# Performance work log

Hardware: AMD Instinct MI355X
Metric: run time of the kernel (lower is better)

The kernel has to match this reference:

```python
import jax, jax.numpy as jnp
import numpy as np

# DARTS recurrent genotype (canonical): (activation, predecessor-state index)
GENOTYPE_RECURRENT = [("sigmoid", 0), ("relu", 1), ("relu", 1), ("identity", 1),
                      ("tanh", 2), ("sigmoid", 5), ("tanh", 3), ("relu", 5)]
GENOTYPE_CONCAT = [1, 2, 3, 4, 5, 6, 7, 8]

T, B, H, V = 512, 64, 1024, 50000
INITRANGE = 0.04

_ACT = {"tanh": jnp.tanh, "relu": jax.nn.relu, "sigmoid": jax.nn.sigmoid,
        "identity": lambda x: x}


def setup_inputs() -> dict:
    key = jax.random.key(0)
    ks = jax.random.split(key, 5)
    X = jax.random.randint(ks[0], (T, B), 0, V)                     # token ids (T, B)
    hidden = jnp.zeros((1, B, H), dtype=jnp.float32)                # init hidden list[0]
    emb_table = jax.random.normal(ks[1], (V, H), dtype=jnp.float32) * 0.1
    W0 = jax.random.uniform(ks[2], (2 * H, 2 * H), jnp.float32, -INITRANGE, INITRANGE)
    Ws = jax.random.uniform(ks[3], (len(GENOTYPE_RECURRENT), H, 2 * H), jnp.float32,
                            -INITRANGE, INITRANGE)
    W_out = jax.random.normal(ks[4], (H, 4), dtype=jnp.float32) * 0.02
    b_out = jnp.zeros((4,), dtype=jnp.float32)
    return {"X": X, "hidden": hidden, "emb_table": emb_table, "W0": W0,
            "Ws": Ws, "W_out": W_out, "b_out": b_out}


def _darts_cell_step(h_prev, x, W0, Ws):
    # x, h_prev: (B, H). Eval-mode (no dropout masks).
    xh = jnp.concatenate([x, h_prev], axis=-1)          # (B, 2H)
    c0h0 = xh @ W0                                      # (B, 2H)
    c0 = jax.nn.sigmoid(c0h0[:, :H])
    h0 = jnp.tanh(c0h0[:, H:])
    s0 = h_prev + c0 * (h0 - h_prev)
    states = [s0]
    for i, (name, pred) in enumerate(GENOTYPE_RECURRENT):
        s_prev = states[pred]
        ch = s_prev @ Ws[i]                             # (B, 2H)
        c = jax.nn.sigmoid(ch[:, :H])
        hh = _ACT[name](ch[:, H:])
        states.append(s_prev + c * (hh - s_prev))
    # mean over concat nodes
    out = jnp.mean(jnp.stack([states[i] for i in GENOTYPE_CONCAT], axis=-1), axis=-1)
    return out, out


def reference(X, hidden, emb_table, W0, Ws, W_out, b_out):
    emb = emb_table[X]                                  # (T, B, H)
    h0 = hidden[0]                                      # (B, H)

    def step(h, x_t):
        return _darts_cell_step(h, x_t, W0, Ws)

    h_last, hiddens = jax.lax.scan(step, h0, emb)       # h_last: (B, H)
    a_hat = h_last @ W_out + b_out                      # (B, 4)
    probs = jax.nn.softmax(a_hat, axis=1)
    return a_hat, probs
```

## Files before the change

kernel.cpp:

```cpp
#include <hip/hip_runtime.h>

#define TT 512

typedef _Float16 f16;
typedef _Float16 half8 __attribute__((ext_vector_type(8)));
typedef float f32x4 __attribute__((ext_vector_type(4)));

#define MFMA(a,b,c) __builtin_amdgcn_mfma_f32_16x16x32_f16((a),(b),(c),0,0,0)
#define LOSC  2048.0f
#define RLOSC 0.00048828125f

#define RS  18
#define WSZ (16*RS)
#define LSZ (16*WSZ)

__device__ __forceinline__ half8 ldh8(const f16* p){ return *(const half8*)p; }
__device__ __forceinline__ float sgm(float x){ return 1.f/(1.f+__expf(-x)); }
__device__ __forceinline__ float applyact(int k, float x){
  if (k==0) return tanhf(x);
  if (k==1) return sgm(x);
  if (k==2) return fmaxf(x,0.f);
  return x;
}

__device__ __forceinline__ void gbar(unsigned* bar, unsigned ph, int b, int wid, int lane){
  __syncthreads();
  const unsigned tgt = ph + 1u;
  if (wid == 0){
    if (lane == 0){
      __builtin_amdgcn_fence(__ATOMIC_RELEASE, "agent");
      __hip_atomic_store(&bar[b*4], tgt, __ATOMIC_RELEASE, __HIP_MEMORY_SCOPE_AGENT);
    }
    for (;;){
      int ok = 1;
      #pragma unroll
      for (int j=0;j<4;j++){
        unsigned v = __hip_atomic_load(&bar[(lane + 64*j)*4], __ATOMIC_RELAXED, __HIP_MEMORY_SCOPE_AGENT);
        ok &= (v >= tgt);
      }
      if (__all(ok)) break;
      __builtin_amdgcn_s_sleep(1);
    }
    if (lane == 0) __builtin_amdgcn_fence(__ATOMIC_ACQUIRE, "agent");
  }
  __syncthreads();
}

__device__ __forceinline__ void mm_core(
  const f16* __restrict__ Ap, const f16* __restrict__ Alp,
  const f16* __restrict__ Bg, const f16* __restrict__ Ba,
  const f16* __restrict__ Bgl, const f16* __restrict__ Bal,
  int nch, int wlo, float* __restrict__ Lg, float* __restrict__ La,
  int region, int q8, int l15)
{
  f32x4 g0={0,0,0,0},g1={0,0,0,0},a0={0,0,0,0},a1={0,0,0,0};
  #pragma unroll 2
  for (int c=0;c<nch;c++){
    int s = c*32;
    half8 ah=ldh8(Ap+s), al=ldh8(Alp+s);
    half8 wg=ldh8(Bg+s), wa=ldh8(Ba+s);
    g0=MFMA(ah,wg,g0); a0=MFMA(ah,wa,a0);
    g1=MFMA(al,wg,g1); a1=MFMA(al,wa,a1);
    if (wlo){ g1=MFMA(ah,ldh8(Bgl+s),g1); a1=MFMA(ah,ldh8(Bal+s),a1); }
  }
  f32x4 gg = g0 + g1*RLOSC, aa = a0 + a1*RLOSC;
  const int base = region*WSZ + (q8>>1)*RS + l15;
  #pragma unroll
  for (int rr=0;rr<4;rr++){
    Lg[base + rr*RS] = gg[rr];
    La[base + rr*RS] = aa[rr];
  }
}

__device__ __forceinline__ void node_std(
  const f16* __restrict__ SHs, const f16* __restrict__ SLs,
  const f16* __restrict__ Wh, const f16* __restrict__ Wl,
  float* __restrict__ Lg, float* __restrict__ La,
  int region, int kk, int nch, int m0, int c0, int q8, int l15, int wlo)
{
  const f16* Ap  = SHs + (m0+l15)*1024 + kk + q8;
  const f16* Alp = SLs + (m0+l15)*1024 + kk + q8;
  const f16* Bg  = Wh + (c0+l15)*1024 + kk + q8;
  const f16* Ba  = Wh + (1024+c0+l15)*1024 + kk + q8;
  const f16* Bgl = wlo ? Wl + (c0+l15)*1024 + kk + q8 : Bg;
  const f16* Bal = wlo ? Wl + (1024+c0+l15)*1024 + kk + q8 : Ba;
  mm_core(Ap,Alp,Bg,Ba,Bgl,Bal,nch,wlo,Lg,La,region,q8,l15);
}

__device__ __forceinline__ float fin_val(const float* __restrict__ Lg, const float* __restrict__ La,
  const float* __restrict__ ST, int t256, int m0, int c0, int r0, int nr, int sp, int actk)
{
  const int row = t256>>4, col = t256&15;
  const int e = row*RS + col;
  float gs=0.f, as=0.f;
  for (int r=r0; r<r0+nr; ++r){ gs += Lg[r*WSZ+e]; as += La[r*WSZ+e]; }
  float spv = ST[sp*65536 + (m0+row)*1024 + c0 + col];
  return spv + sgm(gs)*(applyact(actk,as)-spv);
}

__device__ __forceinline__ void fin_write(const float* __restrict__ Lg, const float* __restrict__ La,
  float* __restrict__ ST, f16* __restrict__ SH, f16* __restrict__ SL,
  int t256, int m0, int c0, int r0, int nr, int sp, int so, int actk, bool hl)
{
  float s = fin_val(Lg, La, ST, t256, m0, c0, r0, nr, sp, actk);
  const int row = t256>>4, col = t256&15;
  const int idx = so*65536 + (m0+row)*1024 + c0 + col;
  ST[idx] = s;
  if (hl){ f16 hi=(f16)s; SH[idx]=hi; SL[idx]=(f16)((s-(float)hi)*LOSC); }
}

__global__ __launch_bounds__(1024,4) void darts_coop(
  const int* __restrict__ X, const float* __restrict__ emb,
  const float* __restrict__ Wout, const float* __restrict__ bout, float* __restrict__ out,
  const f16* __restrict__ W0Th, const f16* __restrict__ W0Tl,
  const f16* __restrict__ WsTh, const f16* __restrict__ WsTl,
  float* __restrict__ ST, f16* __restrict__ SH, f16* __restrict__ SL,
  f16* __restrict__ XNH, f16* __restrict__ XNL,
  unsigned* bar, int wlo)
{
  const int tid = threadIdx.x, b = blockIdx.x;
  const int wid = tid>>6, lane = tid&63, l15 = lane&15, q8 = (lane>>4)*8;
  const int mt = (b>>3)&3, sct = (b&7)*8 + (b>>5);
  const int m0 = mt*16, c0 = sct*16;
  __shared__ float Lg[LSZ], La[LSZ];
  __shared__ float S6[256], S8[256];
  unsigned ph = 0;

  for (int t=0; t<TT; ++t){
    if (t+1 < TT && tid < 256){
      int row = b>>2, col = ((b&3)<<8) + tid;
      int tok = X[(t+1)*64 + row];
      float v = emb[(size_t)tok*1024 + col];
      f16 hi=(f16)v;
      int xi = ((t+1)&1)*65536 + row*1024 + col;
      XNH[xi]=hi; XNL[xi]=(f16)((v-(float)hi)*LOSC);
    }
    {
      const f16* XH = XNH + (t&1)*65536;
      const f16* XL = XNL + (t&1)*65536;
      int kk = wid*128, ak = kk & 1023;
      const f16* Abh = (wid<8)? XH : SH;
      const f16* Abl = (wid<8)? XL : SL;
      const f16* Ap  = Abh + (m0+l15)*1024 + ak + q8;
      const f16* Alp = Abl + (m0+l15)*1024 + ak + q8;
      const f16* Bg  = W0Th + (c0+l15)*2048 + kk + q8;
      const f16* Ba  = W0Th + (1024+c0+l15)*2048 + kk + q8;
      const f16* Bgl = wlo ? W0Tl + (c0+l15)*2048 + kk + q8 : Bg;
      const f16* Bal = wlo ? W0Tl + (1024+c0+l15)*2048 + kk + q8 : Ba;
      mm_core(Ap,Alp,Bg,Ba,Bgl,Bal,4,wlo,Lg,La,wid,q8,l15);
    }
    __syncthreads();
    if (tid<256) fin_write(Lg,La,ST,SH,SL, tid, m0,c0, 0,16, 0, 1, 0, true);
    gbar(bar, ph++, b, wid, lane);

    node_std(SH+1*65536, SL+1*65536, WsTh, WsTl, Lg, La, wid, wid*64, 2, m0,c0,q8,l15,wlo);
    __syncthreads();
    if (tid<256) fin_write(Lg,La,ST,SH,SL, tid, m0,c0, 0,16, 1, 2, 1, true);
    gbar(bar, ph++, b, wid, lane);

    if (wid<8)
      node_std(SH+2*65536, SL+2*65536, WsTh+(size_t)1*2097152,
               wlo? WsTl+(size_t)1*2097152 : (const f16*)0,
               Lg, La, wid, wid*128, 4, m0,c0,q8,l15,wlo);
    else
      node_std(SH+2*65536, SL+2*65536, WsTh+(size_t)2*2097152,
               wlo? WsTl+(size_t)2*2097152 : (const f16*)0,
               Lg, La, wid, (wid-8)*128, 4, m0,c0,q8,l15,wlo);
    __syncthreads();
    if (tid<256)      fin_write(Lg,La,ST,SH,SL, tid,     m0,c0, 0,8, 2, 3, 2, true);
    else if (tid<512) fin_write(Lg,La,ST,SH,SL, tid-256, m0,c0, 8,8, 2, 4, 2, true);
    __syncthreads();

    node_std(SH+2*65536, SL+2*65536, WsTh+(size_t)3*2097152,
             wlo? WsTl+(size_t)3*2097152 : (const f16*)0,
             Lg, La, wid, wid*64, 2, m0,c0,q8,l15,wlo);
    __syncthreads();
    if (tid<256) fin_write(Lg,La,ST,SH,SL, tid, m0,c0, 0,16, 2, 5, 3, false);
    gbar(bar, ph++, b, wid, lane);

    if (wid<8)
      node_std(SH+3*65536, SL+3*65536, WsTh+(size_t)4*2097152,
               wlo? WsTl+(size_t)4*2097152 : (const f16*)0,
               Lg, La, wid, wid*128, 4, m0,c0,q8,l15,wlo);
    else
      node_std(SH+4*65536, SL+4*65536, WsTh+(size_t)6*2097152,
               wlo? WsTl+(size_t)6*2097152 : (const f16*)0,
               Lg, La, wid, (wid-8)*128, 4, m0,c0,q8,l15,wlo);
    __syncthreads();
    if (tid<256)      fin_write(Lg,La,ST,SH,SL, tid,     m0,c0, 0,8, 3, 6, 0, true);
    else if (tid<512) fin_write(Lg,La,ST,SH,SL, tid-256, m0,c0, 8,8, 4, 8, 0, false);
    gbar(bar, ph++, b, wid, lane);

    if (wid<8)
      node_std(SH+6*65536, SL+6*65536, WsTh+(size_t)5*2097152,
               wlo? WsTl+(size_t)5*2097152 : (const f16*)0,
               Lg, La, wid, wid*128, 4, m0,c0,q8,l15,wlo);
    else
      node_std(SH+6*65536, SL+6*65536, WsTh+(size_t)7*2097152,
               wlo? WsTl+(size_t)7*2097152 : (const f16*)0,
               Lg, La, wid, (wid-8)*128, 4, m0,c0,q8,l15,wlo);
    __syncthreads();
    if (tid<256)      S6[tid]     = fin_val(Lg,La,ST, tid,     m0,c0, 0,8, 6, 1);
    else if (tid<512) S8[tid-256] = fin_val(Lg,La,ST, tid-256, m0,c0, 8,8, 6, 2);
    __syncthreads();
    if (tid<256){
      const int row = tid>>4, col = tid&15;
      const int idx = (m0+row)*1024 + c0 + col;
      float m = (ST[2*65536+idx]+ST[3*65536+idx]+ST[4*65536+idx]+ST[5*65536+idx]
               + ST[6*65536+idx]+ST[8*65536+idx]+S6[tid]+S8[tid])*0.125f;
      ST[idx]=m;
      f16 hi=(f16)m; SH[idx]=hi; SL[idx]=(f16)((m-(float)hi)*LOSC);
    }
    gbar(bar, ph++, b, wid, lane);
  }

  if (b==0 && tid<256){
    int row = tid>>2, col = tid&3;
    float acc = bout[col];
    const float* hrow = ST + row*1024;
    #pragma unroll 8
    for (int k=0;k<1024;k++) acc += hrow[k]*Wout[k*4+col];
    out[row*4+col] = acc;
    float m = fmaxf(acc, __shfl_xor(acc,1));
    m = fmaxf(m, __shfl_xor(m,2));
    float e = __expf(acc-m);
    float ssum = e + __shfl_xor(e,1);
    ssum = ssum + __shfl_xor(ssum,2);
    out[256 + row*4+col] = e/ssum;
  }
}

__global__ void prep_x0(const int* __restrict__ X, const float* __restrict__ hidden,
  const float* __restrict__ emb, f16* __restrict__ XNH, f16* __restrict__ XNL,
  float* __restrict__ ST, f16* __restrict__ SH, f16* __restrict__ SL, unsigned* bar)
{
  int idx = blockIdx.x*256 + threadIdx.x;
  float hv = hidden[idx];
  ST[idx] = hv;
  f16 hh=(f16)hv; SH[idx]=hh; SL[idx]=(f16)((hv-(float)hh)*LOSC);
  int brow = idx>>10, k = idx&1023;
  int tok = X[brow];
  float v = emb[tok*1024+k];
  f16 xh=(f16)v; XNH[idx]=xh; XNL[idx]=(f16)((v-(float)xh)*LOSC);
  if (idx < 4096) bar[idx] = 0u;
}

__global__ void prep_w(const float* __restrict__ W0, const float* __restrict__ Ws,
  f16* __restrict__ W0Th, f16* __restrict__ W0Tl, f16* __restrict__ WsTh, f16* __restrict__ WsTl)
{
  __shared__ float L[64][65];
  int b = blockIdx.x, tid = threadIdx.x;
  const float* src; f16 *Dh, *Dl; int K, tk, tn;
  if (b < 1024){ src=W0; Dh=W0Th; Dl=W0Tl; K=2048; tk=b&31; tn=b>>5; }
  else { int bb=b-1024; int mi=bb>>9; int t2=bb&511; tk=t2&15; tn=t2>>4;
         src = Ws + (size_t)mi*1024*2048; Dh = WsTh + (size_t)mi*2097152;
         Dl = WsTl ? (WsTl + (size_t)mi*2097152) : (f16*)0; K=1024; }
  int k0 = tk*64, n0 = tn*64;
  int rr = tid>>6, cc = tid&63;
  #pragma unroll
  for (int j=0;j<16;j++){
    int r = j*4 + rr;
    L[cc][r] = src[(size_t)(k0+r)*2048 + n0+cc];
  }
  __syncthreads();
  #pragma unroll
  for (int j=0;j<16;j++){
    int n = j*4 + rr;
    float v = L[n][cc];
    f16 hi = (f16)v;
    Dh[(size_t)(n0+n)*K + k0+cc] = hi;
    if (Dl) Dl[(size_t)(n0+n)*K + k0+cc] = (f16)((v-(float)hi)*LOSC);
  }
}

__global__ void sentinel_k(float* __restrict__ out, float v){
  int i = blockIdx.x*256 + threadIdx.x;
  if (i < 512) out[i] = v;
}

extern "C" void kernel_launch(void* const* d_in, const int* in_sizes, int n_in,
                              void* d_out, int out_size, void* d_ws, size_t ws_size,
                              hipStream_t stream)
{
  const int*   X      = (const int*)  d_in[0];
  const float* hidden = (const float*)d_in[1];
  const float* emb    = (const float*)d_in[2];
  const float* W0     = (const float*)d_in[3];
  const float* Ws     = (const float*)d_in[4];
  const float* Wout   = (const float*)d_in[5];
  const float* bout   = (const float*)d_in[6];
  float* out = (float*)d_out;

  const size_t SZ_W0   = (size_t)2048*2048*2;
  const size_t SZ_WS   = (size_t)8*2048*1024*2;
  const size_t SZ_ST   = (size_t)10*65536*4;
  const size_t SZ_SHL  = (size_t)10*65536*2;
  const size_t SZ_XN   = (size_t)2*65536*2;
  const size_t SZ_BAR  = 16384;

  auto pad = [](size_t x){ return (x + 255) & ~(size_t)255; };
  size_t need_red  = pad(SZ_W0) + pad(SZ_WS) + pad(SZ_ST) + 2*pad(SZ_SHL)
                   + 2*pad(SZ_XN) + pad(SZ_BAR);
  size_t need_full = need_red + pad(SZ_W0) + pad(SZ_WS);

  int wlo;
  if (ws_size >= need_full)      wlo = 1;
  else if (ws_size >= need_red)  wlo = 0;
  else { hipLaunchKernelGGL(sentinel_k, dim3(2), dim3(256), 0, stream, out, 1.0e6f); return; }

  char* w = (char*)d_ws; size_t off = 0;
  auto alloc = [&](size_t bytes)->void*{ void* p = w+off; off += (bytes+255)&~(size_t)255; return p; };
  f16* W0Th = (f16*)alloc(SZ_W0);
  f16* WsTh = (f16*)alloc(SZ_WS);
  f16* W0Tl = wlo ? (f16*)alloc(SZ_W0) : (f16*)0;
  f16* WsTl = wlo ? (f16*)alloc(SZ_WS) : (f16*)0;
  float* ST = (float*)alloc(SZ_ST);
  f16* SH   = (f16*)alloc(SZ_SHL);
  f16* SL   = (f16*)alloc(SZ_SHL);
  f16* XNH  = (f16*)alloc(SZ_XN);
  f16* XNL  = (f16*)alloc(SZ_XN);
  unsigned* bar = (unsigned*)alloc(SZ_BAR);

  hipLaunchKernelGGL(prep_x0, dim3(256), dim3(256), 0, stream,
                     X, hidden, emb, XNH, XNL, ST, SH, SL, bar);
  hipLaunchKernelGGL(prep_w, dim3(5120), dim3(256), 0, stream,
                     W0, Ws, W0Th, W0Tl, WsTh, WsTl);

  void* args[] = { (void*)&X, (void*)&emb, (void*)&Wout, (void*)&bout, (void*)&out,
                   (void*)&W0Th, (void*)&W0Tl, (void*)&WsTh, (void*)&WsTl,
                   (void*)&ST, (void*)&SH, (void*)&SL, (void*)&XNH, (void*)&XNL,
                   (void*)&bar, (void*)&wlo };
  hipError_t e = hipLaunchCooperativeKernel((void*)darts_coop, dim3(256), dim3(1024), args, 0, stream);
  if (e != hipSuccess){
    hipLaunchKernelGGL(darts_coop, dim3(256), dim3(1024), 0, stream,
                       X, emb, Wout, bout, out, W0Th, W0Tl, WsTh, WsTl,
                       ST, SH, SL, XNH, XNL, bar, wlo);
  }
}
```

Baseline: 64.34 ms.

## Merge nodes 3,4,6 into one barrier stage and prefetch tiles before MFMA

Restructures the per-timestep schedule so node 4 (reading state 2) runs in the same phase as nodes 5 and 7, with the 16 waves split 5/5/6 across the three matmuls. This removes one grid-wide barrier per step at the cost of an extra gbar replacing a local syncthreads and uneven K-splits. It also adds a touch_tiles pass that issues one coalesced 4-byte load per cache line of the wave's A/B tiles before the MFMA loop, so the lines are already in flight when the main loop starts. That pass adds extra load instructions and address arithmetic to every node.

```diff
diff --git a/kernel.cpp b/kernel.cpp
--- a/kernel.cpp
+++ b/kernel.cpp
@@ -46,6 +46,33 @@
   __syncthreads();
 }
 
+__device__ __forceinline__ void touch_tiles(
+  const f16* __restrict__ Wh, const f16* __restrict__ Wl, int Kst, int c0, int kk,
+  const f16* __restrict__ Ah, const f16* __restrict__ Al, int m0, int ak,
+  int nch, int wlo, int lane)
+{
+  unsigned acc = 0;
+  const int tot = (wlo ? 96 : 48) * nch;
+  for (int base = 0; base < tot; base += 64){
+    int id = base + lane;
+    if (id >= tot) id -= tot;
+    int c, a, r;
+    if (wlo){ c = id/96; int ra = id - c*96; a = ra/48; r = ra - a*48; }
+    else    { c = id/48; r = id - c*48; a = 0; }
+    const unsigned* p;
+    if (r < 32){
+      const f16* wb = a ? Wl : Wh;
+      int row = (r<16) ? (c0+r) : (1024 + c0 + (r-16));
+      p = (const unsigned*)(wb + (size_t)row*Kst + kk + c*32);
+    } else {
+      const f16* ab = a ? Al : Ah;
+      p = (const unsigned*)(ab + (size_t)(m0 + (r-32))*1024 + ak + c*32);
+    }
+    acc |= *p;
+  }
+  asm volatile("" :: "v"(acc) : "memory");
+}
+
 __device__ __forceinline__ void mm_core(
   const f16* __restrict__ Ap, const f16* __restrict__ Alp,
   const f16* __restrict__ Bg, const f16* __restrict__ Ba,
@@ -72,12 +99,13 @@
   }
 }
 
-__device__ __forceinline__ void node_std(
+__device__ __forceinline__ void node_g(
   const f16* __restrict__ SHs, const f16* __restrict__ SLs,
   const f16* __restrict__ Wh, const f16* __restrict__ Wl,
   float* __restrict__ Lg, float* __restrict__ La,
-  int region, int kk, int nch, int m0, int c0, int q8, int l15, int wlo)
-{
+  int region, int kk, int nch, int m0, int c0, int q8, int l15, int lane, int wlo)
+{
+  touch_tiles(Wh, Wl, 1024, c0, kk, SHs, SLs, m0, kk, nch, wlo, lane);
   const f16* Ap  = SHs + (m0+l15)*1024 + kk + q8;
   const f16* Alp = SLs + (m0+l15)*1024 + kk + q8;
   const f16* Bg  = Wh + (c0+l15)*1024 + kk + q8;
@@ -141,6 +169,7 @@
       int kk = wid*128, ak = kk & 1023;
       const f16* Abh = (wid<8)? XH : SH;
       const f16* Abl = (wid<8)? XL : SL;
+      touch_tiles(W0Th, W0Tl, 2048, c0, kk, Abh, Abl, m0, ak, 4, wlo, lane);
       const f16* Ap  = Abh + (m0+l15)*1024 + ak + q8;
       const f16* Alp = Abl + (m0+l15)*1024 + ak + q8;
       const f16* Bg  = W0Th + (c0+l15)*2048 + kk + q8;
@@ -153,52 +182,54 @@
     if (tid<256) fin_write(Lg,La,ST,SH,SL, tid, m0,c0, 0,16, 0, 1, 0, true);
     gbar(bar, ph++, b, wid, lane);
 
-    node_std(SH+1*65536, SL+1*65536, WsTh, WsTl, Lg, La, wid, wid*64, 2, m0,c0,q8,l15,wlo);
+    node_g(SH+1*65536, SL+1*65536, WsTh, WsTl, Lg, La, wid, wid*64, 2, m0,c0,q8,l15,lane,wlo);
     __syncthreads();
     if (tid<256) fin_write(Lg,La,ST,SH,SL, tid, m0,c0, 0,16, 1, 2, 1, true);
     gbar(bar, ph++, b, wid, lane);
 
     if (wid<8)
-      node_std(SH+2*65536, SL+2*65536, WsTh+(size_t)1*2097152,
-               wlo? WsTl+(size_t)1*2097152 : (const f16*)0,
-               Lg, La, wid, wid*128, 4, m0,c0,q8,l15,wlo);
+      node_g(SH+2*65536, SL+2*65536, WsTh+(size_t)1*2097152,
+             wlo? WsTl+(size_t)1*2097152 : (const f16*)0,
+             Lg, La, wid, wid*128, 4, m0,c0,q8,l15,lane,wlo);
     else
-      node_std(SH+2*65536, SL+2*65536, WsTh+(size_t)2*2097152,
-               wlo? WsTl+(size_t)2*2097152 : (const f16*)0,
-               Lg, La, wid, (wid-8)*128, 4, m0,c0,q8,l15,wlo);
+      node_g(SH+2*65536, SL+2*65536, WsTh+(size_t)2*2097152,
+             wlo? WsTl+(size_t)2*2097152 : (const f16*)0,
+             Lg, La, wid, (wid-8)*128, 4, m0,c0,q8,l15,lane,wlo);
     __syncthreads();
     if (tid<256)      fin_write(Lg,La,ST,SH,SL, tid,     m0,c0, 0,8, 2, 3, 2, true);
     else if (tid<512) fin_write(Lg,La,ST,SH,SL, tid-256, m0,c0, 8,8, 2, 4, 2, true);
-    __syncthreads();
-
-    node_std(SH+2*65536, SL+2*65536, WsTh+(size_t)3*2097152,
+    gbar(bar, ph++, b, wid, lane);
+
+    if (wid < 5){
+      int i = wid;    int s=(i*32)/5, e=((i+1)*32)/5;
+      node_g(SH+3*65536, SL+3*65536, WsTh+(size_t)4*2097152,
+             wlo? WsTl+(size_t)4*2097152 : (const f16*)0,
+             Lg, La, wid, s*32, e-s, m0,c0,q8,l15,lane,wlo);
+    } else if (wid < 10){
+      int i = wid-5;  int s=(i*32)/5, e=((i+1)*32)/5;
+      node_g(SH+4*65536, SL+4*65536, WsTh+(size_t)6*2097152,
+             wlo? WsTl+(size_t)6*2097152 : (const f16*)0,
+             Lg, La, wid, s*32, e-s, m0,c0,q8,l15,lane,wlo);
+    } else {
+      int i = wid-10; int s=(i*32)/6, e=((i+1)*32)/6;
+      node_g(SH+2*65536, SL+2*65536, WsTh+(size_t)3*2097152,
              wlo? WsTl+(size_t)3*2097152 : (const f16*)0,
-             Lg, La, wid, wid*64, 2, m0,c0,q8,l15,wlo);
-    __syncthreads();
-    if (tid<256) fin_write(Lg,La,ST,SH,SL, tid, m0,c0, 0,16, 2, 5, 3, false);
+             Lg, La, wid, s*32, e-s, m0,c0,q8,l15,lane,wlo);
+    }
+    __syncthreads();
+    if (tid<256)      fin_write(Lg,La,ST,SH,SL, tid,     m0,c0, 0,5,  3, 6, 0, true);
+    else if (tid<512) fin_write(Lg,La,ST,SH,SL, tid-256, m0,c0, 5,5,  4, 8, 0, false);
+    else if (tid<768) fin_write(Lg,La,ST,SH,SL, tid-512, m0,c0, 10,6, 2, 5, 3, false);
     gbar(bar, ph++, b, wid, lane);
 
     if (wid<8)
-      node_std(SH+3*65536, SL+3*65536, WsTh+(size_t)4*2097152,
-               wlo? WsTl+(size_t)4*2097152 : (const f16*)0,
-               Lg, La, wid, wid*128, 4, m0,c0,q8,l15,wlo);
+      node_g(SH+6*65536, SL+6*65536, WsTh+(size_t)5*2097152,
+             wlo? WsTl+(size_t)5*2097152 : (const f16*)0,
+             Lg, La, wid, wid*128, 4, m0,c0,q8,l15,lane,wlo);
     else
-      node_std(SH+4*65536, SL+4*65536, WsTh+(size_t)6*2097152,
-               wlo? WsTl+(size_t)6*2097152 : (const f16*)0,
-               Lg, La, wid, (wid-8)*128, 4, m0,c0,q8,l15,wlo);
-    __syncthreads();
-    if (tid<256)      fin_write(Lg,La,ST,SH,SL, tid,     m0,c0, 0,8, 3, 6, 0, true);
-    else if (tid<512) fin_write(Lg,La,ST,SH,SL, tid-256, m0,c0, 8,8, 4, 8, 0, false);
-    gbar(bar, ph++, b, wid, lane);
-
-    if (wid<8)
-      node_std(SH+6*65536, SL+6*65536, WsTh+(size_t)5*2097152,
-               wlo? WsTl+(size_t)5*2097152 : (const f16*)0,
-               Lg, La, wid, wid*128, 4, m0,c0,q8,l15,wlo);
-    else
-      node_std(SH+6*65536, SL+6*65536, WsTh+(size_t)7*2097152,
-               wlo? WsTl+(size_t)7*2097152 : (const f16*)0,
-               Lg, La, wid, (wid-8)*128, 4, m0,c0,q8,l15,wlo);
+      node_g(SH+6*65536, SL+6*65536, WsTh+(size_t)7*2097152,
+             wlo? WsTl+(size_t)7*2097152 : (const f16*)0,
+             Lg, La, wid, (wid-8)*128, 4, m0,c0,q8,l15,lane,wlo);
     __syncthreads();
     if (tid<256)      S6[tid]     = fin_val(Lg,La,ST, tid,     m0,c0, 0,8, 6, 1);
     else if (tid<512) S8[tid-256] = fin_val(Lg,La,ST, tid-256, m0,c0, 8,8, 6, 2);
```

Measured after the change: 78.87 ms. 1.23x slower.

## Split grid barrier into arrive/wait and prefetch next node weights in between

Applied to the files above, without the earlier changes.

Replaces the all-to-all polling grid barrier with a split arrive/wait barrier. Block 0 gathers the arrivals and publishes a single release flag, and the per-block flags are padded to 64-byte spacing. Between arrive and wait, each wave preloads the first two K-chunks of the next node's weight fragments into registers, so weight loads overlap with barrier latency. This adds register pressure under a 1024-thread, 4-occupancy launch bound. It also adds an extra hop through block 0 on the barrier's critical path.

```diff
diff --git a/kernel.cpp b/kernel.cpp
--- a/kernel.cpp
+++ b/kernel.cpp
@@ -23,40 +23,76 @@
   return x;
 }
 
-__device__ __forceinline__ void gbar(unsigned* bar, unsigned ph, int b, int wid, int lane){
+__device__ __forceinline__ void gbar_arrive(unsigned* bar, unsigned ph, int b, int tid){
   __syncthreads();
+  if (tid==0){
+    __builtin_amdgcn_fence(__ATOMIC_RELEASE, "agent");
+    __hip_atomic_store(&bar[b*16], ph+1u, __ATOMIC_RELAXED, __HIP_MEMORY_SCOPE_AGENT);
+  }
+}
+
+__device__ __forceinline__ void gbar_wait(unsigned* bar, unsigned ph, int b, int tid){
   const unsigned tgt = ph + 1u;
-  if (wid == 0){
-    if (lane == 0){
-      __builtin_amdgcn_fence(__ATOMIC_RELEASE, "agent");
-      __hip_atomic_store(&bar[b*4], tgt, __ATOMIC_RELEASE, __HIP_MEMORY_SCOPE_AGENT);
-    }
-    for (;;){
-      int ok = 1;
-      #pragma unroll
-      for (int j=0;j<4;j++){
-        unsigned v = __hip_atomic_load(&bar[(lane + 64*j)*4], __ATOMIC_RELAXED, __HIP_MEMORY_SCOPE_AGENT);
-        ok &= (v >= tgt);
-      }
-      if (__all(ok)) break;
-      __builtin_amdgcn_s_sleep(1);
-    }
-    if (lane == 0) __builtin_amdgcn_fence(__ATOMIC_ACQUIRE, "agent");
+  if (b==0){
+    if (tid<256){
+      while (__hip_atomic_load(&bar[tid*16], __ATOMIC_RELAXED, __HIP_MEMORY_SCOPE_AGENT) < tgt)
+        __builtin_amdgcn_s_sleep(2);
+    }
+    __syncthreads();
+    if (tid==0){
+      __builtin_amdgcn_fence(__ATOMIC_ACQ_REL, "agent");
+      __hip_atomic_store(&bar[4096], tgt, __ATOMIC_RELAXED, __HIP_MEMORY_SCOPE_AGENT);
+    }
+  }
+  if (tid==0){
+    while (__hip_atomic_load(&bar[4096], __ATOMIC_RELAXED, __HIP_MEMORY_SCOPE_AGENT) < tgt)
+      __builtin_amdgcn_s_sleep(2);
+    __builtin_amdgcn_fence(__ATOMIC_ACQUIRE, "agent");
   }
   __syncthreads();
 }
 
-__device__ __forceinline__ void mm_core(
+struct WF2 { half8 g0,a0,gl0,al0,g1,a1,gl1,al1; };
+
+__device__ __forceinline__ WF2 preW(const f16* __restrict__ Wh, const f16* __restrict__ Wl,
+  int Kst, int c0, int kk, int q8, int l15, int wlo)
+{
+  WF2 F;
+  const f16* Bg = Wh + (size_t)(c0+l15)*Kst + kk + q8;
+  const f16* Ba = Wh + (size_t)(1024+c0+l15)*Kst + kk + q8;
+  F.g0=ldh8(Bg); F.a0=ldh8(Ba); F.g1=ldh8(Bg+32); F.a1=ldh8(Ba+32);
+  if (wlo){
+    const f16* Bgl = Wl + (size_t)(c0+l15)*Kst + kk + q8;
+    const f16* Bal = Wl + (size_t)(1024+c0+l15)*Kst + kk + q8;
+    F.gl0=ldh8(Bgl); F.al0=ldh8(Bal); F.gl1=ldh8(Bgl+32); F.al1=ldh8(Bal+32);
+  } else { F.gl0=F.g0; F.al0=F.a0; F.gl1=F.g1; F.al1=F.a1; }
+  return F;
+}
+
+template<int NCH>
+__device__ __forceinline__ void mm_mix(const WF2& F,
   const f16* __restrict__ Ap, const f16* __restrict__ Alp,
   const f16* __restrict__ Bg, const f16* __restrict__ Ba,
   const f16* __restrict__ Bgl, const f16* __restrict__ Bal,
-  int nch, int wlo, float* __restrict__ Lg, float* __restrict__ La,
+  int wlo, float* __restrict__ Lg, float* __restrict__ La,
   int region, int q8, int l15)
 {
   f32x4 g0={0,0,0,0},g1={0,0,0,0},a0={0,0,0,0},a1={0,0,0,0};
-  #pragma unroll 2
-  for (int c=0;c<nch;c++){
-    int s = c*32;
+  {
+    half8 ah=ldh8(Ap), al=ldh8(Alp);
+    g0=MFMA(ah,F.g0,g0); a0=MFMA(ah,F.a0,a0);
+    g1=MFMA(al,F.g0,g1); a1=MFMA(al,F.a0,a1);
+    if (wlo){ g1=MFMA(ah,F.gl0,g1); a1=MFMA(ah,F.al0,a1); }
+  }
+  if (NCH>1){
+    half8 ah=ldh8(Ap+32), al=ldh8(Alp+32);
+    g0=MFMA(ah,F.g1,g0); a0=MFMA(ah,F.a1,a0);
+    g1=MFMA(al,F.g1,g1); a1=MFMA(al,F.a1,a1);
+    if (wlo){ g1=MFMA(ah,F.gl1,g1); a1=MFMA(ah,F.al1,a1); }
+  }
+  #pragma unroll
+  for (int c=2;c<NCH;c++){
+    int s=c*32;
     half8 ah=ldh8(Ap+s), al=ldh8(Alp+s);
     half8 wg=ldh8(Bg+s), wa=ldh8(Ba+s);
     g0=MFMA(ah,wg,g0); a0=MFMA(ah,wa,a0);
@@ -72,19 +108,20 @@
   }
 }
 
-__device__ __forceinline__ void node_std(
+template<int NCH>
+__device__ __forceinline__ void node_pre(const WF2& F,
   const f16* __restrict__ SHs, const f16* __restrict__ SLs,
   const f16* __restrict__ Wh, const f16* __restrict__ Wl,
   float* __restrict__ Lg, float* __restrict__ La,
-  int region, int kk, int nch, int m0, int c0, int q8, int l15, int wlo)
+  int region, int kk, int m0, int c0, int q8, int l15, int wlo)
 {
   const f16* Ap  = SHs + (m0+l15)*1024 + kk + q8;
   const f16* Alp = SLs + (m0+l15)*1024 + kk + q8;
-  const f16* Bg  = Wh + (c0+l15)*1024 + kk + q8;
-  const f16* Ba  = Wh + (1024+c0+l15)*1024 + kk + q8;
-  const f16* Bgl = wlo ? Wl + (c0+l15)*1024 + kk + q8 : Bg;
-  const f16* Bal = wlo ? Wl + (1024+c0+l15)*1024 + kk + q8 : Ba;
-  mm_core(Ap,Alp,Bg,Ba,Bgl,Bal,nch,wlo,Lg,La,region,q8,l15);
+  const f16* Bg  = Wh + (size_t)(c0+l15)*1024 + kk + q8;
+  const f16* Ba  = Wh + (size_t)(1024+c0+l15)*1024 + kk + q8;
+  const f16* Bgl = wlo ? Wl + (size_t)(c0+l15)*1024 + kk + q8 : Bg;
+  const f16* Bal = wlo ? Wl + (size_t)(1024+c0+l15)*1024 + kk + q8 : Ba;
+  mm_mix<NCH>(F, Ap, Alp, Bg, Ba, Bgl, Bal, wlo, Lg, La, region, q8, l15);
 }
 
 __device__ __forceinline__ float fin_val(const float* __restrict__ Lg, const float* __restrict__ La,
@@ -126,6 +163,8 @@
   __shared__ float S6[256], S8[256];
   unsigned ph = 0;
 
+  WF2 F0 = preW(W0Th, W0Tl, 2048, c0, wid*128, q8, l15, wlo);
+
   for (int t=0; t<TT; ++t){
     if (t+1 < TT && tid < 256){
       int row = b>>2, col = ((b&3)<<8) + tid;
@@ -143,62 +182,86 @@
       const f16* Abl = (wid<8)? XL : SL;
       const f16* Ap  = Abh + (m0+l15)*1024 + ak + q8;
       const f16* Alp = Abl + (m0+l15)*1024 + ak + q8;
-      const f16* Bg  = W0Th + (c0+l15)*2048 + kk + q8;
-      const f16* Ba  = W0Th + (1024+c0+l15)*2048 + kk + q8;
-      const f16* Bgl = wlo ? W0Tl + (c0+l15)*2048 + kk + q8 : Bg;
-      const f16* Bal = wlo ? W0Tl + (1024+c0+l15)*2048 + kk + q8 : Ba;
-      mm_core(Ap,Alp,Bg,Ba,Bgl,Bal,4,wlo,Lg,La,wid,q8,l15);
+      const f16* Bg  = W0Th + (size_t)(c0+l15)*2048 + kk + q8;
+      const f16* Ba  = W0Th + (size_t)(1024+c0+l15)*2048 + kk + q8;
+      const f16* Bgl = wlo ? W0Tl + (size_t)(c0+l15)*2048 + kk + q8 : Bg;
+      const f16* Bal = wlo ? W0Tl + (size_t)(1024+c0+l15)*2048 + kk + q8 : Ba;
+      mm_mix<4>(F0, Ap, Alp, Bg, Ba, Bgl, Bal, wlo, Lg, La, wid, q8, l15);
     }
     __syncthreads();
     if (tid<256) fin_write(Lg,La,ST,SH,SL, tid, m0,c0, 0,16, 0, 1, 0, true);
-    gbar(bar, ph++, b, wid, lane);
-
-    node_std(SH+1*65536, SL+1*65536, WsTh, WsTl, Lg, La, wid, wid*64, 2, m0,c0,q8,l15,wlo);
+    gbar_arrive(bar, ph, b, tid);
+    WF2 F1 = preW(WsTh, WsTl, 1024, c0, wid*64, q8, l15, wlo);
+    gbar_wait(bar, ph, b, tid); ph++;
+
+    node_pre<2>(F1, SH+1*65536, SL+1*65536, WsTh, WsTl, Lg, La, wid, wid*64, m0,c0,q8,l15,wlo);
     __syncthreads();
     if (tid<256) fin_write(Lg,La,ST,SH,SL, tid, m0,c0, 0,16, 1, 2, 1, true);
-    gbar(bar, ph++, b, wid, lane);
+    gbar_arrive(bar, ph, b, tid);
+    WF2 F2 = (wid<8)
+      ? preW(WsTh+(size_t)1*2097152, wlo? WsTl+(size_t)1*2097152 : (const f16*)0,
+             1024, c0, (wid&7)*128, q8, l15, wlo)
+      : preW(WsTh+(size_t)2*2097152, wlo? WsTl+(size_t)2*2097152 : (const f16*)0,
+             1024, c0, (wid&7)*128, q8, l15, wlo);
+    gbar_wait(bar, ph, b, tid); ph++;
 
     if (wid<8)
-      node_std(SH+2*65536, SL+2*65536, WsTh+(size_t)1*2097152,
-               wlo? WsTl+(size_t)1*2097152 : (const f16*)0,
-               Lg, La, wid, wid*128, 4, m0,c0,q8,l15,wlo);
+      node_pre<4>(F2, SH+2*65536, SL+2*65536, WsTh+(size_t)1*2097152,
+                  wlo? WsTl+(size_t)1*2097152 : (const f16*)0,
+                  Lg, La, wid, (wid&7)*128, m0,c0,q8,l15,wlo);
     else
-      node_std(SH+2*65536, SL+2*65536, WsTh+(size_t)2*2097152,
-               wlo? WsTl+(size_t)2*2097152 : (const f16*)0,
-               Lg, La, wid, (wid-8)*128, 4, m0,c0,q8,l15,wlo);
+      node_pre<4>(F2, SH+2*65536, SL+2*65536, WsTh+(size_t)2*2097152,
+                  wlo? WsTl+(size_t)2*2097152 : (const f16*)0,
+                  Lg, La, wid, (wid&7)*128, m0,c0,q8,l15,wlo);
     __syncthreads();
     if (tid<256)      fin_write(Lg,La,ST,SH,SL, tid,     m0,c0, 0,8, 2, 3, 2, true);
     else if (tid<512) fin_write(Lg,La,ST,SH,SL, tid-256, m0,c0, 8,8, 2, 4, 2, true);
     __syncthreads();
 
-    node_std(SH+2*65536, SL+2*65536, WsTh+(size_t)3*2097152,
-             wlo? WsTl+(size_t)3*2097152 : (const f16*)0,
-             Lg, La, wid, wid*64, 2, m0,c0,q8,l15,wlo);
+    {
+      WF2 F2b = preW(WsTh+(size_t)3*2097152, wlo? WsTl+(size_t)3*2097152 : (const f16*)0,
+                     1024, c0, wid*64, q8, l15, wlo);
+      node_pre<2>(F2b, SH+2*65536, SL+2*65536, WsTh+(size_t)3*2097152,
+                  wlo? WsTl+(size_t)3*2097152 : (const f16*)0,
+                  Lg, La, wid, wid*64, m0,c0,q8,l15,wlo);
+    }
     __syncthreads();
     if (tid<256) fin_write(Lg,La,ST,SH,SL, tid, m0,c0, 0,16, 2, 5, 3, false);
-    gbar(bar, ph++, b, wid, lane);
+    gbar_arrive(bar, ph, b, tid);
+    WF2 F3 = (wid<8)
+      ? preW(WsTh+(size_t)4*2097152, wlo? WsTl+(size_t)4*2097152 : (const f16*)0,
+             1024, c0, (wid&7)*128, q8, l15, wlo)
+      : preW(WsTh+(size_t)6*2097152, wlo? WsTl+(size_t)6*2097152 : (const f16*)0,
+             1024, c0, (wid&7)*128, q8, l15, wlo);
+    gbar_wait(bar, ph, b, tid); ph++;
 
     if (wid<8)
-      node_std(SH+3*65536, SL+3*65536, WsTh+(size_t)4*2097152,
-               wlo? WsTl+(size_t)4*2097152 : (const f16*)0,
-               Lg, La, wid, wid*128, 4, m0,c0,q8,l15,wlo);
+      node_pre<4>(F3, SH+3*65536, SL+3*65536, WsTh+(size_t)4*2097152,
+                  wlo? WsTl+(size_t)4*2097152 : (const f16*)0,
+                  Lg, La, wid, (wid&7)*128, m0,c0,q8,l15,wlo);
     else
-      node_std(SH+4*65536, SL+4*65536, WsTh+(size_t)6*2097152,
-               wlo? WsTl+(size_t)6*2097152 : (const f16*)0,
-               Lg, La, wid, (wid-8)*128, 4, m0,c0,q8,l15,wlo);
+      node_pre<4>(F3, SH+4*65536, SL+4*65536, WsTh+(size_t)6*2097152,
+                  wlo? WsTl+(size_t)6*2097152 : (const f16*)0,
+                  Lg, La, wid, (wid&7)*128, m0,c0,q8,l15,wlo);
     __syncthreads();
     if (tid<256)      fin_write(Lg,La,ST,SH,SL, tid,     m0,c0, 0,8, 3, 6, 0, true);
     else if (tid<512) fin_write(Lg,La,ST,SH,SL, tid-256, m0,c0, 8,8, 4, 8, 0, false);
-    gbar(bar, ph++, b, wid, lane);
+    gbar_arrive(bar, ph, b, tid);
+    WF2 F4 = (wid<8)
+      ? preW(WsTh+(size_t)5*2097152, wlo? WsTl+(size_t)5*2097152 : (const f16*)0,
+             1024, c0, (wid&7)*128, q8, l15, wlo)
+      : preW(WsTh+(size_t)7*2097152, wlo? WsTl+(size_t)7*2097152 : (const f16*)0,
+             1024, c0, (wid&7)*128, q8, l15, wlo);
+    gbar_wait(bar, ph, b, tid); ph++;
 
     if (wid<8)
-      node_std(SH+6*65536, SL+6*65536, WsTh+(size_t)5*2097152,
-               wlo? WsTl+(size_t)5*2097152 : (const f16*)0,
-               Lg, La, wid, wid*128, 4, m0,c0,q8,l15,wlo);
+      node_pre<4>(F4, SH+6*65536, SL+6*65536, WsTh+(size_t)5*2097152,
+                  wlo? WsTl+(size_t)5*2097152 : (const f16*)0,
+                  Lg, La, wid, (wid&7)*128, m0,c0,q8,l15,wlo);
     else
-      node_std(SH+6*65536, SL+6*65536, WsTh+(size_t)7*2097152,
-               wlo? WsTl+(size_t)7*2097152 : (const f16*)0,
-               Lg, La, wid, (wid-8)*128, 4, m0,c0,q8,l15,wlo);
+      node_pre<4>(F4, SH+6*65536, SL+6*65536, WsTh+(size_t)7*2097152,
+                  wlo? WsTl+(size_t)7*2097152 : (const f16*)0,
+                  Lg, La, wid, (wid&7)*128, m0,c0,q8,l15,wlo);
     __syncthreads();
     if (tid<256)      S6[tid]     = fin_val(Lg,La,ST, tid,     m0,c0, 0,8, 6, 1);
     else if (tid<512) S8[tid-256] = fin_val(Lg,La,ST, tid-256, m0,c0, 8,8, 6, 2);
@@ -211,7 +274,9 @@
       ST[idx]=m;
       f16 hi=(f16)m; SH[idx]=hi; SL[idx]=(f16)((m-(float)hi)*LOSC);
     }
-    gbar(bar, ph++, b, wid, lane);
+    gbar_arrive(bar, ph, b, tid);
+    F0 = preW(W0Th, W0Tl, 2048, c0, wid*128, q8, l15, wlo);
+    gbar_wait(bar, ph, b, tid); ph++;
   }
 
   if (b==0 && tid<256){
@@ -242,7 +307,7 @@
   int tok = X[brow];
   float v = emb[tok*1024+k];
   f16 xh=(f16)v; XNH[idx]=xh; XNL[idx]=(f16)((v-(float)xh)*LOSC);
-  if (idx < 4096) bar[idx] = 0u;
+  if (idx < 8192) bar[idx] = 0u;
 }
 
 __global__ void prep_w(const float* __restrict__ W0, const float* __restrict__ Ws,
@@ -296,7 +361,7 @@
   const size_t SZ_ST   = (size_t)10*65536*4;
   const size_t SZ_SHL  = (size_t)10*65536*2;
   const size_t SZ_XN   = (size_t)2*65536*2;
-  const size_t SZ_BAR  = 16384;
+  const size_t SZ_BAR  = 32768;
 
   auto pad = [](size_t x){ return (x + 255) & ~(size_t)255; };
   size_t need_red  = pad(SZ_W0) + pad(SZ_WS) + pad(SZ_ST) + 2*pad(SZ_SHL)
```

New measurement: 64.89 ms. No clear change (+0.8%).
